# Performance work log

Measured on AMD Instinct MI355X. Metric: run time of the kernel, lower is better.

The kernel has to match this reference:

```python
import jax, jax.numpy as jnp
import numpy as np

STATE_BITS = 10          # L: bits of trellis state
SHIFT_BITS = 2           # K: bits shifted in per step -> 2^K predecessors
CHUNK = 4                # chunk_size: values emitted per trellis step
S = 1 << STATE_BITS      # number of states (codebook rows)
NPRED = 1 << SHIFT_BITS  # predecessors per state
HI = 1 << (STATE_BITS - SHIFT_BITS)


def setup_inputs() -> dict:
    key = jax.random.key(0)
    k1, k2 = jax.random.split(key)
    array = jax.random.normal(k1, (1024, 1024), dtype=jnp.float32)
    codebook = jax.random.normal(k2, (S, CHUNK), dtype=jnp.float32)
    return {"array": array, "codebook": codebook, "block_size": 16}


def _viterbi(x, codebook):
    # x: [T, CHUNK, B] target chunks; codebook: [S, CHUNK]
    # Exact min-squared-error Viterbi over the bit-shift trellis:
    #   next_state = ((prev << K) | new_bits) mod 2^L
    # Predecessors of state s: (s >> K) + j * 2^(L-K), j in [0, 2^K)
    s = jnp.arange(S)
    prev_idx = (s[:, None] >> SHIFT_BITS) + jnp.arange(NPRED)[None, :] * HI  # [S, NPRED]
    cnorm = jnp.sum(codebook * codebook, axis=1)  # [S]

    def cost(xt):  # xt: [CHUNK, B] -> [S, B] squared distances
        return cnorm[:, None] - 2.0 * (codebook @ xt) + jnp.sum(xt * xt, axis=0)[None, :]

    alpha0 = cost(x[0])  # free initial state: cost of emitting first chunk

    def step(alpha, xt):
        cand = alpha[prev_idx]                        # [S, NPRED, B]
        j = jnp.argmin(cand, axis=1)                  # [S, B]
        alpha_new = jnp.min(cand, axis=1) + cost(xt)  # [S, B]
        return alpha_new, j.astype(jnp.int8)

    alpha_T, bps = jax.lax.scan(step, alpha0, x[1:])  # bps: [T-1, S, B] int8
    last = jnp.argmin(alpha_T, axis=0).astype(jnp.int32)  # [B] state at step T-1

    def back(state, bp):
        # state: [B] state at step t; bp: [S, B] backpointers into step t
        j = jnp.take_along_axis(bp, state[None, :], axis=0)[0].astype(jnp.int32)
        prev = (state >> SHIFT_BITS) + j * HI
        return prev, state

    first, rest = jax.lax.scan(back, last, bps, reverse=True)
    return jnp.concatenate([first[None], rest], axis=0)  # [T, B] int32


def reference(array, codebook, block_size):
    rows, columns = array.shape
    br, bc = rows // block_size, columns // block_size
    epb = block_size * block_size          # elements_per_block
    T = epb // CHUNK                       # number_of_steps
    B = br * bc                            # number_of_blocks
    # block reshape: [rows, cols] -> [elements_per_block, number_of_blocks]
    blocks = (array.reshape(br, block_size, bc, block_size)
                   .transpose(0, 2, 1, 3)
                   .reshape(B, epb).T)
    x = blocks.reshape(T, CHUNK, B)
    states = _viterbi(x, codebook)         # [T, B]
    vals = codebook[states]                # [T, B, CHUNK] gather reconstruct
    rec = vals.transpose(0, 2, 1).reshape(epb, B)
    rec = (rec.T.reshape(br, bc, block_size, block_size)
              .transpose(0, 2, 1, 3)
              .reshape(rows, columns))
    states_out = states.T.reshape(br, bc, T)
    return rec, states_out
```

## Files before the change

### kernel.cpp

```cpp
#include <hip/hip_runtime.h>


#define COLS      1024
#define T_STEPS   64
#define REC_SIZE  (1024 * 1024)

__global__ __launch_bounds__(256)
__attribute__((amdgpu_waves_per_eu(4, 4)))
void viterbi_q(
    const float* __restrict__ arr,
    const float* __restrict__ cbook,
    float* __restrict__ out)
{
    const int tid   = threadIdx.x;
    const int wid   = tid >> 6;
    const int lane  = tid & 63;
    const int chain = (blockIdx.x << 2) | wid;
    const int rb    = chain >> 6;
    const int cb    = chain & 63;

    __shared__ __align__(16) float tile[4][256];
    __shared__ __align__(16) float Mst[4][256];
    __shared__ unsigned char Jb[4][63 * 64];
    __shared__ int st_lds[4][64];

    {
        const int r  = lane >> 2;
        const int c4 = (lane & 3) << 2;
        float4 v = *(const float4*)(arr + (rb * 16 + r) * COLS + cb * 16 + c4);
        *(float4*)&tile[wid][lane << 2] = v;
    }
    *(float4*)&Mst[wid][lane << 2] = make_float4(0.f, 0.f, 0.f, 0.f);

    float4 a[16];
    float  h[16];
    #pragma unroll
    for (int j = 0; j < 4; ++j) {
        #pragma unroll
        for (int c = 0; c < 4; ++c) {
            const int row = (lane << 2) + c + (j << 8);
            float4 v = *(const float4*)(cbook + row * 4);
            a[j * 4 + c] = v;
            h[j * 4 + c] = -0.5f * (v.x * v.x + v.y * v.y +
                                    v.z * v.z + v.w * v.w);
        }
    }
    #pragma unroll
    for (int j = 0; j < 4; ++j) {
        asm volatile(""
            : "+v"(a[j*4+0].x), "+v"(a[j*4+0].y), "+v"(a[j*4+0].z), "+v"(a[j*4+0].w),
              "+v"(a[j*4+1].x), "+v"(a[j*4+1].y), "+v"(a[j*4+1].z), "+v"(a[j*4+1].w),
              "+v"(a[j*4+2].x), "+v"(a[j*4+2].y), "+v"(a[j*4+2].z), "+v"(a[j*4+2].w),
              "+v"(a[j*4+3].x), "+v"(a[j*4+3].y), "+v"(a[j*4+3].z), "+v"(a[j*4+3].w),
              "+v"(h[j*4+0]), "+v"(h[j*4+1]), "+v"(h[j*4+2]), "+v"(h[j*4+3]));
    }

    const float* __restrict__ tilep = &tile[wid][0];
    float* __restrict__ Mp          = &Mst[wid][0];
    unsigned char* __restrict__ Jp  = &Jb[wid][0];

    #pragma unroll 1
    for (int t = 0; t < T_STEPS - 1; ++t) {
        float4 xt = *(const float4*)&tilep[t << 2];
        float mj[4];
        #pragma unroll
        for (int j = 0; j < 4; ++j)
            mj[j] = Mp[lane + 64 * j];

        float nm[4];
        unsigned bp = 0;
        #pragma unroll
        for (int c = 0; c < 4; ++c) {
            float cand[4];
            #pragma unroll
            for (int j = 0; j < 4; ++j) {
                const float4 av = a[j * 4 + c];
                float acc = fmaf(av.x, xt.x, h[j * 4 + c]);
                acc = fmaf(av.y, xt.y, acc);
                acc = fmaf(av.z, xt.z, acc);
                acc = fmaf(av.w, xt.w, acc);
                cand[j] = acc + mj[j];
            }
            const float v = fmaxf(fmaxf(cand[0], cand[1]),
                                  fmaxf(cand[2], cand[3]));
            const int j = (cand[0] == v) ? 0
                        : (cand[1] == v) ? 1
                        : (cand[2] == v) ? 2 : 3;
            nm[c] = v;
            bp |= (unsigned)j << (2 * c);
        }
        *(float4*)&Mp[lane << 2] = make_float4(nm[0], nm[1], nm[2], nm[3]);
        Jp[t * 64 + lane] = (unsigned char)bp;
    }

    int bests;
    {
        const int t = T_STEPS - 1;
        float4 xt = *(const float4*)&tilep[t << 2];
        float mj[4];
        #pragma unroll
        for (int j = 0; j < 4; ++j)
            mj[j] = Mp[lane + 64 * j];

        float bv = -3.4e38f;
        int   bs = 0;
        #pragma unroll
        for (int j = 0; j < 4; ++j) {
            #pragma unroll
            for (int c = 0; c < 4; ++c) {
                const float4 av = a[j * 4 + c];
                float acc = fmaf(av.x, xt.x, h[j * 4 + c]);
                acc = fmaf(av.y, xt.y, acc);
                acc = fmaf(av.z, xt.z, acc);
                acc = fmaf(av.w, xt.w, acc);
                acc += mj[j];
                if (acc > bv) { bv = acc; bs = (lane << 2) + c + (j << 8); }
            }
        }
        #pragma unroll
        for (int off = 32; off > 0; off >>= 1) {
            const float ov = __shfl_xor(bv, off, 64);
            const int   os = __shfl_xor(bs, off, 64);
            if (ov > bv || (ov == bv && os < bs)) { bv = ov; bs = os; }
        }
        bests = bs;
    }

    if (lane == 0) {
        int s = bests;
        st_lds[wid][T_STEPS - 1] = s;
        for (int i = T_STEPS - 2; i >= 0; --i) {
            const int p = s >> 2;
            const unsigned byte = Jp[i * 64 + (p >> 2)];
            const int j = (byte >> (2 * (p & 3))) & 3;
            s = p + (j << 8);
            st_lds[wid][i] = s;
        }
    }
    __syncthreads();

    const int st = st_lds[wid][lane];
    out[REC_SIZE + chain * 64 + lane] = (float)st;
    const float4 v = *(const float4*)(cbook + st * 4);
    const int r  = lane >> 2;
    const int c4 = (lane & 3) << 2;
    *(float4*)(out + (rb * 16 + r) * COLS + cb * 16 + c4) = v;
}

extern "C" void kernel_launch(void* const* d_in, const int* in_sizes, int n_in,
                              void* d_out, int out_size, void* d_ws, size_t ws_size,
                              hipStream_t stream)
{
    const float* arr   = (const float*)d_in[0];
    const float* cbook = (const float*)d_in[1];
    float* out = (float*)d_out;
    viterbi_q<<<dim3(1024), dim3(256), 0, stream>>>(arr, cbook, out);
}
```

Before: 105.9 us.

## Split each Viterbi chain across two waves with double-buffered LDS metrics

Each 16x16 block's trellis is now processed by a 128-thread workgroup (two wavefronts) instead of one wavefront, with each thread handling two states per predecessor group rather than four. The path metrics become double-buffered in LDS, a workgroup barrier is added every step, and backpointers are packed as nibble pairs across two steps. The final argmax is reduced across the two waves through shared memory. This halves per-thread register and ALU work per step to shorten the serial recurrence and raise occupancy, at the cost of 63 barriers per chain and four times as many workgroups.

```diff
diff --git a/kernel.cpp b/kernel.cpp
--- a/kernel.cpp
+++ b/kernel.cpp
@@ -5,9 +5,7 @@
 #define T_STEPS   64
 #define REC_SIZE  (1024 * 1024)
 
-__global__ __launch_bounds__(256)
-__attribute__((amdgpu_waves_per_eu(4, 4)))
-void viterbi_q(
+__global__ __launch_bounds__(128) void viterbi_q(
     const float* __restrict__ arr,
     const float* __restrict__ cbook,
     float* __restrict__ out)
@@ -15,70 +13,67 @@
     const int tid   = threadIdx.x;
     const int wid   = tid >> 6;
     const int lane  = tid & 63;
-    const int chain = (blockIdx.x << 2) | wid;
+    const int chain = blockIdx.x;
     const int rb    = chain >> 6;
-    const int cb    = chain & 63;
+    const int cbc   = chain & 63;
 
-    __shared__ __align__(16) float tile[4][256];
-    __shared__ __align__(16) float Mst[4][256];
-    __shared__ unsigned char Jb[4][63 * 64];
-    __shared__ int st_lds[4][64];
+    __shared__ __align__(16) float tile[256];
+    __shared__ __align__(16) float Mbuf[512];
+    __shared__ unsigned char J[32 * 128];
+    __shared__ int   st_lds[64];
+    __shared__ float redv[2];
+    __shared__ int   reds[2];
 
-    {
-        const int r  = lane >> 2;
-        const int c4 = (lane & 3) << 2;
-        float4 v = *(const float4*)(arr + (rb * 16 + r) * COLS + cb * 16 + c4);
-        *(float4*)&tile[wid][lane << 2] = v;
+    if (tid < 64) {
+        const int r  = tid >> 2;
+        const int c4 = (tid & 3) << 2;
+        float4 v = *(const float4*)(arr + (rb * 16 + r) * COLS + cbc * 16 + c4);
+        *(float4*)&tile[tid << 2] = v;
     }
-    *(float4*)&Mst[wid][lane << 2] = make_float4(0.f, 0.f, 0.f, 0.f);
+    *(float2*)&Mbuf[tid << 1] = make_float2(0.f, 0.f);
 
-    float4 a[16];
-    float  h[16];
+    float4 a[8];
+    float  h[8];
     #pragma unroll
     for (int j = 0; j < 4; ++j) {
         #pragma unroll
-        for (int c = 0; c < 4; ++c) {
-            const int row = (lane << 2) + c + (j << 8);
+        for (int c = 0; c < 2; ++c) {
+            const int row = (tid << 1) + c + (j << 8);
             float4 v = *(const float4*)(cbook + row * 4);
-            a[j * 4 + c] = v;
-            h[j * 4 + c] = -0.5f * (v.x * v.x + v.y * v.y +
+            a[j * 2 + c] = v;
+            h[j * 2 + c] = -0.5f * (v.x * v.x + v.y * v.y +
                                     v.z * v.z + v.w * v.w);
         }
     }
-    #pragma unroll
-    for (int j = 0; j < 4; ++j) {
-        asm volatile(""
-            : "+v"(a[j*4+0].x), "+v"(a[j*4+0].y), "+v"(a[j*4+0].z), "+v"(a[j*4+0].w),
-              "+v"(a[j*4+1].x), "+v"(a[j*4+1].y), "+v"(a[j*4+1].z), "+v"(a[j*4+1].w),
-              "+v"(a[j*4+2].x), "+v"(a[j*4+2].y), "+v"(a[j*4+2].z), "+v"(a[j*4+2].w),
-              "+v"(a[j*4+3].x), "+v"(a[j*4+3].y), "+v"(a[j*4+3].z), "+v"(a[j*4+3].w),
-              "+v"(h[j*4+0]), "+v"(h[j*4+1]), "+v"(h[j*4+2]), "+v"(h[j*4+3]));
-    }
+    __syncthreads();
 
-    const float* __restrict__ tilep = &tile[wid][0];
-    float* __restrict__ Mp          = &Mst[wid][0];
-    unsigned char* __restrict__ Jp  = &Jb[wid][0];
+    const int pg = tid >> 1;
+    unsigned nib_hold = 0;
 
     #pragma unroll 1
     for (int t = 0; t < T_STEPS - 1; ++t) {
-        float4 xt = *(const float4*)&tilep[t << 2];
+        const float* __restrict__ Mr = Mbuf + ((t & 1) << 8);
+        float* __restrict__       Mw = Mbuf + (((t + 1) & 1) << 8);
+
+        float4 xt = *(const float4*)&tile[t << 2];
         float mj[4];
         #pragma unroll
         for (int j = 0; j < 4; ++j)
-            mj[j] = Mp[lane + 64 * j];
+            mj[j] = Mr[pg + 64 * j];
 
-        float nm[4];
+        float nm[2];
         unsigned bp = 0;
         #pragma unroll
-        for (int c = 0; c < 4; ++c) {
+        for (int c = 0; c < 2; ++c) {
             float cand[4];
             #pragma unroll
             for (int j = 0; j < 4; ++j) {
-                const float4 av = a[j * 4 + c];
-                float acc = fmaf(av.x, xt.x, h[j * 4 + c]);
+                const float4 av = a[j * 2 + c];
+                float acc = fmaf(av.x, xt.x, h[j * 2 + c]);
                 acc = fmaf(av.y, xt.y, acc);
                 acc = fmaf(av.z, xt.z, acc);
                 acc = fmaf(av.w, xt.w, acc);
+                cand[c ? 4 + j - 4 : j] = acc + mj[j];
                 cand[j] = acc + mj[j];
             }
             const float v = fmaxf(fmaxf(cand[0], cand[1]),
@@ -89,32 +84,34 @@
             nm[c] = v;
             bp |= (unsigned)j << (2 * c);
         }
-        *(float4*)&Mp[lane << 2] = make_float4(nm[0], nm[1], nm[2], nm[3]);
-        Jp[t * 64 + lane] = (unsigned char)bp;
+        *(float2*)&Mw[tid << 1] = make_float2(nm[0], nm[1]);
+        if (t & 1) J[(t >> 1) * 128 + tid] = (unsigned char)(nib_hold | (bp << 4));
+        else       nib_hold = bp;
+        __syncthreads();
     }
+    J[31 * 128 + tid] = (unsigned char)nib_hold;
 
-    int bests;
     {
-        const int t = T_STEPS - 1;
-        float4 xt = *(const float4*)&tilep[t << 2];
+        const float* __restrict__ Mr = Mbuf + ((63 & 1) << 8);
+        float4 xt = *(const float4*)&tile[63 << 2];
         float mj[4];
         #pragma unroll
         for (int j = 0; j < 4; ++j)
-            mj[j] = Mp[lane + 64 * j];
+            mj[j] = Mr[pg + 64 * j];
 
         float bv = -3.4e38f;
         int   bs = 0;
         #pragma unroll
         for (int j = 0; j < 4; ++j) {
             #pragma unroll
-            for (int c = 0; c < 4; ++c) {
-                const float4 av = a[j * 4 + c];
-                float acc = fmaf(av.x, xt.x, h[j * 4 + c]);
+            for (int c = 0; c < 2; ++c) {
+                const float4 av = a[j * 2 + c];
+                float acc = fmaf(av.x, xt.x, h[j * 2 + c]);
                 acc = fmaf(av.y, xt.y, acc);
                 acc = fmaf(av.z, xt.z, acc);
                 acc = fmaf(av.w, xt.w, acc);
                 acc += mj[j];
-                if (acc > bv) { bv = acc; bs = (lane << 2) + c + (j << 8); }
+                if (acc > bv) { bv = acc; bs = (tid << 1) + c + (j << 8); }
             }
         }
         #pragma unroll
@@ -123,28 +120,37 @@
             const int   os = __shfl_xor(bs, off, 64);
             if (ov > bv || (ov == bv && os < bs)) { bv = ov; bs = os; }
         }
-        bests = bs;
+        if (lane == 0) { redv[wid] = bv; reds[wid] = bs; }
     }
+    __syncthreads();
 
-    if (lane == 0) {
-        int s = bests;
-        st_lds[wid][T_STEPS - 1] = s;
+    if (tid == 0) {
+        float bv = redv[0]; int bs = reds[0];
+        if (redv[1] > bv || (redv[1] == bv && reds[1] < bs)) {
+            bv = redv[1]; bs = reds[1];
+        }
+        int s = bs;
+        st_lds[T_STEPS - 1] = s;
         for (int i = T_STEPS - 2; i >= 0; --i) {
             const int p = s >> 2;
-            const unsigned byte = Jp[i * 64 + (p >> 2)];
-            const int j = (byte >> (2 * (p & 3))) & 3;
+            const unsigned byte = J[(i >> 1) * 128 + (p >> 1)];
+            const int j = (byte >> (((i & 1) << 2) + ((p & 1) << 1))) & 3;
             s = p + (j << 8);
-            st_lds[wid][i] = s;
+            st_lds[i] = s;
         }
     }
     __syncthreads();
 
-    const int st = st_lds[wid][lane];
-    out[REC_SIZE + chain * 64 + lane] = (float)st;
-    const float4 v = *(const float4*)(cbook + st * 4);
-    const int r  = lane >> 2;
-    const int c4 = (lane & 3) << 2;
-    *(float4*)(out + (rb * 16 + r) * COLS + cb * 16 + c4) = v;
+    if (tid < 64) {
+        const int st = st_lds[tid];
+        const float4 v = *(const float4*)(cbook + st * 4);
+        const int r  = tid >> 2;
+        const int c4 = (tid & 3) << 2;
+        *(float4*)(out + (rb * 16 + r) * COLS + cbc * 16 + c4) = v;
+    } else {
+        const int t = tid - 64;
+        out[REC_SIZE + chain * 64 + t] = (float)st_lds[t];
+    }
 }
 
 extern "C" void kernel_launch(void* const* d_in, const int* in_sizes, int n_in,
@@ -154,5 +160,5 @@
     const float* arr   = (const float*)d_in[0];
     const float* cbook = (const float*)d_in[1];
     float* out = (float*)d_out;
-    viterbi_q<<<dim3(1024), dim3(256), 0, stream>>>(arr, cbook, out);
+    viterbi_q<<<dim3(4096), dim3(128), 0, stream>>>(arr, cbook, out);
 }
```

Result: no change. 107.7 us (+1.7%).
